# Optimization experiments

Measured on AMD Instinct MI355X. Metric: run time of the kernel, lower is better.

The kernel has to match this reference:

```python
import jax, jax.numpy as jnp
import numpy as np

N_NODES = 500000
N_EDGES = 1000000
D = 32            # unconcat_embed_dim
CD = 2 * D        # concat feature width (node/edge feats into InnerGNN)
HID = 2 * CD      # InnerGNN hidden
RBF_CENTERS = jnp.arange(0.0, 2.0, 0.1, dtype=jnp.float32)  # 20 centers
RBF_GAMMA = 10.0
VOCAB_DIR, VOCAB_TYPE, VOCAB_RING = 8, 16, 4


def setup_inputs() -> dict:
    key = jax.random.key(0)
    ks = jax.random.split(key, 20)
    inp = {
        "atom_repr": jax.random.normal(ks[0], (N_NODES, CD), dtype=jnp.float32),
        "src": jax.random.randint(ks[1], (N_EDGES,), 0, N_NODES, dtype=jnp.int32),
        "dst": jax.random.randint(ks[2], (N_EDGES,), 0, N_NODES, dtype=jnp.int32),
        "r_dir": jax.random.randint(ks[3], (N_EDGES,), 0, VOCAB_DIR, dtype=jnp.int32),
        "r_type": jax.random.randint(ks[4], (N_EDGES,), 0, VOCAB_TYPE, dtype=jnp.int32),
        "r_ring": jax.random.randint(ks[5], (N_EDGES,), 0, VOCAB_RING, dtype=jnp.int32),
        "p_dir": jax.random.randint(ks[6], (N_EDGES,), 0, VOCAB_DIR, dtype=jnp.int32),
        "p_type": jax.random.randint(ks[7], (N_EDGES,), 0, VOCAB_TYPE, dtype=jnp.int32),
        "p_ring": jax.random.randint(ks[8], (N_EDGES,), 0, VOCAB_RING, dtype=jnp.int32),
        "r_len": jax.random.uniform(ks[9], (N_EDGES,), dtype=jnp.float32, maxval=2.0),
        "p_len": jax.random.uniform(ks[10], (N_EDGES,), dtype=jnp.float32, maxval=2.0),
        # learned params
        "emb_dir": jax.random.normal(ks[11], (VOCAB_DIR, D), dtype=jnp.float32) * 0.02,
        "emb_type": jax.random.normal(ks[12], (VOCAB_TYPE, D), dtype=jnp.float32) * 0.02,
        "emb_ring": jax.random.normal(ks[13], (VOCAB_RING, D), dtype=jnp.float32) * 0.02,
        "rbf_W": jax.random.normal(ks[14], (RBF_CENTERS.shape[0], D), dtype=jnp.float32) * 0.1,
        "rbf_b": jnp.zeros((D,), dtype=jnp.float32),
        "W1": jax.random.normal(ks[15], (CD, HID), dtype=jnp.float32) * (1.0 / np.sqrt(CD)),
        "b1": jnp.zeros((HID,), dtype=jnp.float32),
        "W2": jax.random.normal(ks[16], (HID, CD), dtype=jnp.float32) * (1.0 / np.sqrt(HID)),
        "b2": jnp.zeros((CD,), dtype=jnp.float32),
    }
    return inp


def _bond_embed(d, t, r, length, emb_dir, emb_type, emb_ring, rbf_W, rbf_b):
    # categorical embeddings summed over features + RBF-expanded bond length
    cat = emb_dir[d] + emb_type[t] + emb_ring[r]                       # [E, D]
    rbf = jnp.exp(-RBF_GAMMA * (length[:, None] - RBF_CENTERS) ** 2)   # [E, 20]
    return cat + rbf @ rbf_W + rbf_b                                   # [E, D]


def reference(atom_repr, src, dst, r_dir, r_type, r_ring, p_dir, p_type, p_ring,
              r_len, p_len, emb_dir, emb_type, emb_ring, rbf_W, rbf_b,
              W1, b1, W2, b2):
    r_embed = _bond_embed(r_dir, r_type, r_ring, r_len, emb_dir, emb_type, emb_ring, rbf_W, rbf_b)
    p_embed = _bond_embed(p_dir, p_type, p_ring, p_len, emb_dir, emb_type, emb_ring, rbf_W, rbf_b)
    concat_bond = jnp.concatenate([r_embed, p_embed - r_embed], axis=1)  # [E, CD]
    # InnerGNN: gather src node feats, add edge feats, sum-aggregate at dst, MLP
    msg = atom_repr[src] + concat_bond                                   # [E, CD]
    agg = jax.ops.segment_sum(msg, dst, num_segments=atom_repr.shape[0]) # [N, CD]
    h = jax.nn.relu(agg @ W1 + b1)
    out = jax.nn.relu(h @ W2 + b2)  # has_last_act=True; dropout is identity (eval)
    return out
```

## Files before the change

kernel.cpp:

```cpp
#include <hip/hip_runtime.h>


#define CD 64
#define HID 128

__global__ __launch_bounds__(256) void transpose_w1_kernel(
    const float* __restrict__ W1,
    float* __restrict__ W1t)
{
    int idx = blockIdx.x * 256 + threadIdx.x;
    if (idx >= 64 * 128) return;
    int i = idx >> 7;
    int j = idx & 127;
    W1t[j * 64 + i] = W1[i * 128 + j];
}

__global__ __launch_bounds__(256) void edge_kernel(
    const float* __restrict__ atom,
    const int*   __restrict__ srcv, const int* __restrict__ dstv,
    const int*   __restrict__ rdv,  const int* __restrict__ rtv, const int* __restrict__ rrv,
    const int*   __restrict__ pdv,  const int* __restrict__ ptv, const int* __restrict__ prv,
    const float* __restrict__ rlenv, const float* __restrict__ plenv,
    const float* __restrict__ Edir,
    const float* __restrict__ Etyp,
    const float* __restrict__ Erng,
    const float* __restrict__ rbfW,
    const float* __restrict__ rbfB,
    float* __restrict__ agg,
    int nE)
{
    int e = blockIdx.x * 4 + (threadIdx.x >> 6);
    if (e >= nE) return;
    e = __builtin_amdgcn_readfirstlane(e);

    int  f    = threadIdx.x & 63;
    int  d    = f & 31;
    bool rhalf = (f < 32);

    int   s  = srcv[e];
    int   t  = dstv[e];

    int   id = rhalf ? rdv[e]  : pdv[e];
    int   it = rhalf ? rtv[e]  : ptv[e];
    int   ir = rhalf ? rrv[e]  : prv[e];
    float L  = rhalf ? rlenv[e] : plenv[e];

    float cat = Edir[id * 32 + d] + Etyp[it * 32 + d] + Erng[ir * 32 + d];

    float A = expf(-10.f * L * L);
    float T = expf(2.f * L);

    const float Bk[20] = {
        1.0f,            9.0483742e-1f,  6.7032005e-1f,  4.0656966e-1f,
        2.0189652e-1f,   8.2084999e-2f,  2.7323722e-2f,  7.4465830e-3f,
        1.6615573e-3f,   3.0353914e-4f,  4.5399930e-5f,  5.5595310e-6f,
        5.5739037e-7f,   4.5753326e-8f,  3.0748799e-9f,  1.6918798e-10f,
        7.6217622e-12f,  2.8111856e-13f, 8.4885308e-15f, 2.0984571e-16f
    };

    float p = 1.f, acc = 0.f;
#pragma unroll
    for (int k = 0; k < 20; ++k) {
        acc = fmaf(p, Bk[k] * rbfW[k * 32 + d], acc);
        p *= T;
    }
    float mine = cat + A * acc;

    float other = __shfl_xor(mine, 32, 64);
    float val = rhalf ? (mine + rbfB[d])
                      : (mine - other);

    float msg = atom[(size_t)s * CD + f] + val;
    atomicAdd(&agg[(size_t)t * CD + f], msg);
}

__global__ __launch_bounds__(256) void mlp_kernel(
    const float* __restrict__ W1t,
    const float* __restrict__ b1,
    const float* __restrict__ W2,
    const float* __restrict__ b2,
    float* __restrict__ io,
    int nN)
{
    int n = blockIdx.x * 256 + threadIdx.x;
    if (n >= nN) return;
    float* row = io + (size_t)n * CD;

    float a[CD];
#pragma unroll
    for (int i = 0; i < CD / 4; ++i) {
        float4 v = reinterpret_cast<const float4*>(row)[i];
        a[4 * i + 0] = v.x; a[4 * i + 1] = v.y;
        a[4 * i + 2] = v.z; a[4 * i + 3] = v.w;
    }

    float acc[CD];
#pragma unroll
    for (int o = 0; o < CD; ++o) acc[o] = b2[o];

#pragma unroll 2
    for (int j = 0; j < HID; ++j) {
        const float* w1c = W1t + j * CD;
        float h0 = b1[j], h1 = 0.f, h2 = 0.f, h3 = 0.f;
#pragma unroll
        for (int i = 0; i < CD / 4; ++i) {
            h0 = fmaf(a[4 * i + 0], w1c[4 * i + 0], h0);
            h1 = fmaf(a[4 * i + 1], w1c[4 * i + 1], h1);
            h2 = fmaf(a[4 * i + 2], w1c[4 * i + 2], h2);
            h3 = fmaf(a[4 * i + 3], w1c[4 * i + 3], h3);
        }
        float h = fmaxf((h0 + h1) + (h2 + h3), 0.f);

        const float* w2r = W2 + j * CD;
#pragma unroll
        for (int o = 0; o < CD; ++o) acc[o] = fmaf(h, w2r[o], acc[o]);
    }

#pragma unroll
    for (int i = 0; i < CD / 4; ++i) {
        float4 v;
        v.x = fmaxf(acc[4 * i + 0], 0.f);
        v.y = fmaxf(acc[4 * i + 1], 0.f);
        v.z = fmaxf(acc[4 * i + 2], 0.f);
        v.w = fmaxf(acc[4 * i + 3], 0.f);
        reinterpret_cast<float4*>(row)[i] = v;
    }
}

extern "C" void kernel_launch(void* const* d_in, const int* in_sizes, int n_in,
                              void* d_out, int out_size, void* d_ws, size_t ws_size,
                              hipStream_t stream) {
    const float* atom  = (const float*)d_in[0];
    const int*   srcv  = (const int*)d_in[1];
    const int*   dstv  = (const int*)d_in[2];
    const int*   rdv   = (const int*)d_in[3];
    const int*   rtv   = (const int*)d_in[4];
    const int*   rrv   = (const int*)d_in[5];
    const int*   pdv   = (const int*)d_in[6];
    const int*   ptv   = (const int*)d_in[7];
    const int*   prv   = (const int*)d_in[8];
    const float* rlenv = (const float*)d_in[9];
    const float* plenv = (const float*)d_in[10];
    const float* Edir  = (const float*)d_in[11];
    const float* Etyp  = (const float*)d_in[12];
    const float* Erng  = (const float*)d_in[13];
    const float* rbfW  = (const float*)d_in[14];
    const float* rbfB  = (const float*)d_in[15];
    const float* W1    = (const float*)d_in[16];
    const float* b1    = (const float*)d_in[17];
    const float* W2    = (const float*)d_in[18];
    const float* b2    = (const float*)d_in[19];

    int nE = in_sizes[1];
    int nN = in_sizes[0] / CD;

    float* agg = (float*)d_out;
    float* W1t = (float*)d_ws;

    hipMemsetAsync(agg, 0, (size_t)nN * CD * sizeof(float), stream);

    transpose_w1_kernel<<<32, 256, 0, stream>>>(W1, W1t);

    edge_kernel<<<(nE + 3) / 4, 256, 0, stream>>>(
        atom, srcv, dstv, rdv, rtv, rrv, pdv, ptv, prv, rlenv, plenv,
        Edir, Etyp, Erng, rbfW, rbfB, agg, nE);

    mlp_kernel<<<(nN + 255) / 256, 256, 0, stream>>>(W1t, b1, W2, b2, agg, nN);
}
```

Measured before the change: 1.040 ms.

## Make edge kernel persistent with hoisted RBF weights and split polynomial chains

The edge kernel becomes persistent: a fixed grid of 2048 blocks, with each wavefront processing a contiguous range of edges. The per-lane RBF weight products and the bias are hoisted into registers once per wavefront instead of being reloaded for every edge. The 20-term polynomial is split into two interleaved chains to shorten the dependency latency, and fast __expf replaces expf. Fewer wavefronts in flight may reduce latency hiding for the random gathers and atomics, and __expf may slightly change numerics.

Measured after the change: 865.4 us. 1.2x faster.

```diff
diff --git a/kernel.cpp b/kernel.cpp
--- a/kernel.cpp
+++ b/kernel.cpp
@@ -29,26 +29,11 @@
     float* __restrict__ agg,
     int nE)
 {
-    int e = blockIdx.x * 4 + (threadIdx.x >> 6);
-    if (e >= nE) return;
-    e = __builtin_amdgcn_readfirstlane(e);
-
-    int  f    = threadIdx.x & 63;
-    int  d    = f & 31;
+    int wid = __builtin_amdgcn_readfirstlane(blockIdx.x * 4 + (threadIdx.x >> 6));
+    int nw  = gridDim.x * 4;
+    int f   = threadIdx.x & 63;
+    int d   = f & 31;
     bool rhalf = (f < 32);
-
-    int   s  = srcv[e];
-    int   t  = dstv[e];
-
-    int   id = rhalf ? rdv[e]  : pdv[e];
-    int   it = rhalf ? rtv[e]  : ptv[e];
-    int   ir = rhalf ? rrv[e]  : prv[e];
-    float L  = rhalf ? rlenv[e] : plenv[e];
-
-    float cat = Edir[id * 32 + d] + Etyp[it * 32 + d] + Erng[ir * 32 + d];
-
-    float A = expf(-10.f * L * L);
-    float T = expf(2.f * L);
 
     const float Bk[20] = {
         1.0f,            9.0483742e-1f,  6.7032005e-1f,  4.0656966e-1f,
@@ -58,20 +43,49 @@
         7.6217622e-12f,  2.8111856e-13f, 8.4885308e-15f, 2.0984571e-16f
     };
 
-    float p = 1.f, acc = 0.f;
+    float wkx[10], wky[10];
 #pragma unroll
-    for (int k = 0; k < 20; ++k) {
-        acc = fmaf(p, Bk[k] * rbfW[k * 32 + d], acc);
-        p *= T;
+    for (int m = 0; m < 10; ++m) {
+        wkx[m] = Bk[2 * m]     * rbfW[(2 * m) * 32 + d];
+        wky[m] = Bk[2 * m + 1] * rbfW[(2 * m + 1) * 32 + d];
     }
-    float mine = cat + A * acc;
+    float bias = rbfB[d];
 
-    float other = __shfl_xor(mine, 32, 64);
-    float val = rhalf ? (mine + rbfB[d])
-                      : (mine - other);
+    int per = (nE + nw - 1) / nw;
+    int beg = wid * per;
+    int end = beg + per; if (end > nE) end = nE;
 
-    float msg = atom[(size_t)s * CD + f] + val;
-    atomicAdd(&agg[(size_t)t * CD + f], msg);
+    for (int e = beg; e < end; ++e) {
+        int   s  = srcv[e];
+        int   t  = dstv[e];
+        int   id = rhalf ? rdv[e]   : pdv[e];
+        int   it = rhalf ? rtv[e]   : ptv[e];
+        int   ir = rhalf ? rrv[e]   : prv[e];
+        float L  = rhalf ? rlenv[e] : plenv[e];
+
+        float cat = Edir[id * 32 + d] + Etyp[it * 32 + d] + Erng[ir * 32 + d];
+
+        float A  = __expf(-10.f * L * L);
+        float T  = __expf(2.f * L);
+        float T2 = T * T;
+        float px = A, py = A * T;
+        float ax = 0.f, ay = 0.f;
+#pragma unroll
+        for (int m = 0; m < 10; ++m) {
+            ax = fmaf(px, wkx[m], ax);
+            ay = fmaf(py, wky[m], ay);
+            px *= T2;
+            py *= T2;
+        }
+        float mine = cat + ax + ay;
+
+        float other = __shfl_xor(mine, 32);
+        float val = rhalf ? (mine + bias)
+                          : (mine - other);
+
+        float msg = atom[(size_t)s * CD + f] + val;
+        atomicAdd(&agg[(size_t)t * CD + f], msg);
+    }
 }
 
 __global__ __launch_bounds__(256) void mlp_kernel(
@@ -100,20 +114,20 @@
 
 #pragma unroll 2
     for (int j = 0; j < HID; ++j) {
-        const float* w1c = W1t + j * CD;
+        const float* w1 = W1t + (size_t)j * CD;
         float h0 = b1[j], h1 = 0.f, h2 = 0.f, h3 = 0.f;
 #pragma unroll
         for (int i = 0; i < CD / 4; ++i) {
-            h0 = fmaf(a[4 * i + 0], w1c[4 * i + 0], h0);
-            h1 = fmaf(a[4 * i + 1], w1c[4 * i + 1], h1);
-            h2 = fmaf(a[4 * i + 2], w1c[4 * i + 2], h2);
-            h3 = fmaf(a[4 * i + 3], w1c[4 * i + 3], h3);
+            h0 = fmaf(a[4 * i + 0], w1[4 * i + 0], h0);
+            h1 = fmaf(a[4 * i + 1], w1[4 * i + 1], h1);
+            h2 = fmaf(a[4 * i + 2], w1[4 * i + 2], h2);
+            h3 = fmaf(a[4 * i + 3], w1[4 * i + 3], h3);
         }
         float h = fmaxf((h0 + h1) + (h2 + h3), 0.f);
 
-        const float* w2r = W2 + j * CD;
+        const float* w2 = W2 + (size_t)j * CD;
 #pragma unroll
-        for (int o = 0; o < CD; ++o) acc[o] = fmaf(h, w2r[o], acc[o]);
+        for (int o = 0; o < CD; ++o) acc[o] = fmaf(h, w2[o], acc[o]);
     }
 
 #pragma unroll
@@ -157,11 +171,11 @@
     float* agg = (float*)d_out;
     float* W1t = (float*)d_ws;
 
-    hipMemsetAsync(agg, 0, (size_t)nN * CD * sizeof(float), stream);
+    (void)hipMemsetAsync(agg, 0, (size_t)nN * CD * sizeof(float), stream);
 
     transpose_w1_kernel<<<32, 256, 0, stream>>>(W1, W1t);
 
-    edge_kernel<<<(nE + 3) / 4, 256, 0, stream>>>(
+    edge_kernel<<<2048, 256, 0, stream>>>(
         atom, srcv, dstv, rdv, rtv, rrv, pdv, ptv, prv, rlenv, plenv,
         Edir, Etyp, Erng, rbfW, rbfB, agg, nE);
 
```
